# Kernel tuning notes

Measured on AMD Instinct MI355X. Metric: run time of the kernel, lower is better.

## Reference

```python
import jax, jax.numpy as jnp
import numpy as np

GROUP_SIZE = 7
ROI_SCALE = 1.3
BIN_SCALE = 1.5


def setup_inputs() -> dict:
    key = jax.random.key(0)
    k1, k2, k3, k4 = jax.random.split(key, 4)
    B, C, H, W = 2, 490, 128, 128  # C = output_dim(10) * group_size(7)**2
    N = 512
    stride = 16
    features = jax.random.normal(k1, (B, C, H, W), dtype=jnp.float32)
    img_w = W * stride
    bidx = jax.random.randint(k2, (N, 1), 0, B).astype(jnp.float32)
    xy1 = jax.random.uniform(k3, (N, 2), minval=0.0, maxval=img_w - 64.0)
    wh = jax.random.uniform(k4, (N, 2), minval=32.0, maxval=512.0)
    xy2 = jnp.minimum(xy1 + wh, img_w - 1.0)
    rois = jnp.concatenate([bidx, xy1[:, 0:1], xy1[:, 1:2], xy2[:, 0:1], xy2[:, 1:2]], axis=1)
    return {"rois": rois, "features": features, "stride": stride}


def reference(rois, features, stride):
    G = GROUP_SIZE
    B, C, H, W = features.shape
    D = C // (G * G)  # output_dim, computed dynamically as in the torch module
    dt = features.dtype
    spatial_scale = 1.0 / stride

    rois = rois[:, :5].astype(dt)
    batch_idx = rois[:, 0].astype(jnp.int32)  # [N]
    # rounded roi corners in feature-map coordinates (end is inclusive +1)
    rsw = jnp.round(rois[:, 1]) * spatial_scale
    rsh = jnp.round(rois[:, 2]) * spatial_scale
    rew = (jnp.round(rois[:, 3]) + 1.0) * spatial_scale
    reh = (jnp.round(rois[:, 4]) + 1.0) * spatial_scale
    # mask (context) enlargement around roi center by ROI_SCALE
    rw, rh = rew - rsw, reh - rsh
    rwm, rhm = rw * ROI_SCALE, rh * ROI_SCALE
    swm = (rsw + rew) * 0.5 - rwm * 0.5
    shm = (rsh + reh) * 0.5 - rhm * 0.5
    rwm = jnp.maximum(rwm, 0.1)  # force tiny rois to 1x1
    rhm = jnp.maximum(rhm, 0.1)
    bin_h = rhm / G  # [N]
    bin_w = rwm / G
    dh = bin_h * (BIN_SCALE - 1.0) * 0.5  # extra bin context
    dw = bin_w * (BIN_SCALE - 1.0) * 0.5

    g = jnp.arange(G, dtype=dt)  # bin index
    hstart = jnp.clip(jnp.floor(shm[:, None] + g[None, :] * bin_h[:, None] - dh[:, None]), 0, H).astype(jnp.int32)  # [N,G]
    hend = jnp.clip(jnp.ceil(shm[:, None] + (g[None, :] + 1.0) * bin_h[:, None] + dh[:, None]), 0, H).astype(jnp.int32)
    wstart = jnp.clip(jnp.floor(swm[:, None] + g[None, :] * bin_w[:, None] - dw[:, None]), 0, W).astype(jnp.int32)
    wend = jnp.clip(jnp.ceil(swm[:, None] + (g[None, :] + 1.0) * bin_w[:, None] + dw[:, None]), 0, W).astype(jnp.int32)

    # integral image so each bin-average is 4 gathers instead of a dynamic loop
    cs = jnp.cumsum(jnp.cumsum(features, axis=2), axis=3)
    S = jnp.pad(cs, ((0, 0), (0, 0), (1, 0), (1, 0)))  # [B,C,H+1,W+1]
    # position-sensitive channel map c = (d*G + ph)*G + pw  <=>  reshape C -> [D,G,G]
    Sr = S.reshape(B, D, G, G, H + 1, W + 1)

    N = rois.shape[0]
    b_ = batch_idx[:, None, None, None]          # [N,1,1,1]
    d_ = jnp.arange(D)[None, :, None, None]      # [1,D,1,1]
    pi = jnp.arange(G)[None, None, :, None]      # [1,1,G,1] (ph)
    pj = jnp.arange(G)[None, None, None, :]      # [1,1,1,G] (pw)
    hs = hstart[:, None, :, None]
    he = hend[:, None, :, None]
    ws = wstart[:, None, None, :]
    we = wend[:, None, None, :]

    total = (Sr[b_, d_, pi, pj, he, we] - Sr[b_, d_, pi, pj, hs, we]
             - Sr[b_, d_, pi, pj, he, ws] + Sr[b_, d_, pi, pj, hs, ws])  # [N,D,G,G]

    area = ((hend - hstart)[:, None, :, None] * (wend - wstart)[:, None, None, :])  # [N,1->D,G,G] via broadcast
    area = jnp.broadcast_to(area, total.shape)
    out = jnp.where(area > 0, total / jnp.maximum(area, 1).astype(dt), jnp.zeros((), dt))
    return out
```

## Files before the change

### kernel.cpp

```cpp
#include <hip/hip_runtime.h>

#define GS   7
#define CCH  490
#define HH   128
#define WW   128
#define LDW  132
#define NB   2

__global__ __launch_bounds__(512, 4) void psroi_fused(
    const float* __restrict__ rois,
    const float* __restrict__ feat,
    const int*   __restrict__ stride_p,
    float*       __restrict__ out)
{
#pragma clang fp contract(off)
    __shared__ float S[HH * LDW];

    const int bc = blockIdx.x;
    const int b  = bc / CCH;
    const int c  = bc - b * CCH;
    const float* __restrict__ f = feat + (size_t)bc * (HH * WW);
    const int tid = threadIdx.x;

    {
        const int col = tid & 127;
        const int seg = tid >> 7;
        const int r0  = seg * 32;

        float v[32];
        const float* fp = f + r0 * WW + col;
        #pragma unroll
        for (int i = 0; i < 32; ++i)
            v[i] = fp[i * WW];
        #pragma unroll
        for (int i = 1; i < 32; ++i)
            v[i] += v[i - 1];

        S[seg * LDW + col] = v[31];
        __syncthreads();
        float off = 0.0f;
        if (seg > 0) off += S[0 * LDW + col];
        if (seg > 1) off += S[1 * LDW + col];
        if (seg > 2) off += S[2 * LDW + col];
        __syncthreads();

        float* sp = &S[r0 * LDW + col];
        #pragma unroll
        for (int i = 0; i < 32; ++i)
            sp[i * LDW] = v[i] + off;
    }
    __syncthreads();

    {
        const int row = tid >> 2;
        const int ws_ = tid & 3;
        float* rp = &S[row * LDW + ws_ * 32];

        float u[32];
        #pragma unroll
        for (int i = 0; i < 8; ++i) {
            const float4 q = *(const float4*)&rp[i * 4];
            u[4 * i + 0] = q.x; u[4 * i + 1] = q.y;
            u[4 * i + 2] = q.z; u[4 * i + 3] = q.w;
        }
        #pragma unroll
        for (int i = 1; i < 32; ++i)
            u[i] += u[i - 1];

        const float tot = u[31];
        const float t1 = __shfl_up(tot, 1, 64);
        const float t2 = __shfl_up(tot, 2, 64);
        const float t3 = __shfl_up(tot, 3, 64);
        float off = 0.0f;
        if (ws_ > 0) off += t1;
        if (ws_ > 1) off += t2;
        if (ws_ > 2) off += t3;

        #pragma unroll
        for (int i = 0; i < 8; ++i) {
            float4 q;
            q.x = u[4 * i + 0] + off; q.y = u[4 * i + 1] + off;
            q.z = u[4 * i + 2] + off; q.w = u[4 * i + 3] + off;
            *(float4*)&rp[i * 4] = q;
        }
    }
    __syncthreads();

    {
        const int n = tid;
        const float b_f = rois[n * 5 + 0];
        const int bi = (int)b_f;
        if (bi == b) {
            const float ss = 1.0f / (float)(*stride_p);
            const int d   = c / (GS * GS);
            const int rem = c - d * (GS * GS);
            const int pi  = rem / GS;
            const int pj  = rem - pi * GS;

            const float x1 = rois[n * 5 + 1];
            const float y1 = rois[n * 5 + 2];
            const float x2 = rois[n * 5 + 3];
            const float y2 = rois[n * 5 + 4];

            float rsw = rintf(x1) * ss;
            float rsh = rintf(y1) * ss;
            float rew = (rintf(x2) + 1.0f) * ss;
            float reh = (rintf(y2) + 1.0f) * ss;
            float rwv = rew - rsw;
            float rhv = reh - rsh;
            float rwm = rwv * 1.3f;
            float rhm = rhv * 1.3f;
            float swm = (rsw + rew) * 0.5f - rwm * 0.5f;
            float shm = (rsh + reh) * 0.5f - rhm * 0.5f;
            rwm = fmaxf(rwm, 0.1f);
            rhm = fmaxf(rhm, 0.1f);
            float bin_h = rhm / 7.0f;
            float bin_w = rwm / 7.0f;
            float dh = bin_h * 0.25f;
            float dw = bin_w * 0.25f;

            const float gi = (float)pi;
            const float gj = (float)pj;
            const int hs  = (int)fminf(fmaxf(floorf(shm + gi * bin_h - dh),          0.0f), 128.0f);
            const int he  = (int)fminf(fmaxf(ceilf (shm + (gi + 1.0f) * bin_h + dh), 0.0f), 128.0f);
            const int ws2 = (int)fminf(fmaxf(floorf(swm + gj * bin_w - dw),          0.0f), 128.0f);
            const int we  = (int)fminf(fmaxf(ceilf (swm + (gj + 1.0f) * bin_w + dw), 0.0f), 128.0f);

            const int area = (he - hs) * (we - ws2);
            const float A  = (he > 0 && we  > 0) ? S[(he - 1) * LDW + (we  - 1)] : 0.0f;
            const float Bv = (hs > 0 && we  > 0) ? S[(hs - 1) * LDW + (we  - 1)] : 0.0f;
            const float Cv = (he > 0 && ws2 > 0) ? S[(he - 1) * LDW + (ws2 - 1)] : 0.0f;
            const float Dv = (hs > 0 && ws2 > 0) ? S[(hs - 1) * LDW + (ws2 - 1)] : 0.0f;
            const float total = ((A - Bv) - Cv) + Dv;
            out[(size_t)n * CCH + c] = (area > 0) ? (total / (float)area) : 0.0f;
        }
    }
}

extern "C" void kernel_launch(void* const* d_in, const int* in_sizes, int n_in,
                              void* d_out, int out_size, void* d_ws, size_t ws_size,
                              hipStream_t stream)
{
    const float* rois     = (const float*)d_in[0];
    const float* feat     = (const float*)d_in[1];
    const int*   stride_p = (const int*)d_in[2];
    float*       out      = (float*)d_out;

    dim3 grid(NB * CCH);
    dim3 block(512);
    hipLaunchKernelGGL(psroi_fused, grid, block, 0, stream, rois, feat, stride_p, out);
}
```

Baseline: 98.08 us.

## Make psroi kernel persistent with register prefetch of next channel

```diff
diff --git a/kernel.cpp b/kernel.cpp
--- a/kernel.cpp
+++ b/kernel.cpp
@@ -6,6 +6,8 @@
 #define WW   128
 #define LDW  132
 #define NB   2
+#define NCH  (NB * CCH)
+#define NBLK 512
 
 __global__ __launch_bounds__(512, 4) void psroi_fused(
     const float* __restrict__ rois,
@@ -16,124 +18,138 @@
 #pragma clang fp contract(off)
     __shared__ float S[HH * LDW];
 
-    const int bc = blockIdx.x;
-    const int b  = bc / CCH;
-    const int c  = bc - b * CCH;
-    const float* __restrict__ f = feat + (size_t)bc * (HH * WW);
     const int tid = threadIdx.x;
+    const int col = tid & 127;
+    const int seg = tid >> 7;
+    const int r0  = seg * 32;
+    const int row = tid >> 2;
+    const int ws_ = tid & 3;
 
+    const float ss  = 1.0f / (float)(*stride_p);
+    const float b_f = rois[tid * 5 + 0];
+    const int   bi  = (int)b_f;
+    const float x1  = rois[tid * 5 + 1];
+    const float y1  = rois[tid * 5 + 2];
+    const float x2  = rois[tid * 5 + 3];
+    const float y2  = rois[tid * 5 + 4];
+    float rsw = rintf(x1) * ss;
+    float rsh = rintf(y1) * ss;
+    float rew = (rintf(x2) + 1.0f) * ss;
+    float reh = (rintf(y2) + 1.0f) * ss;
+    float rwm = (rew - rsw) * 1.3f;
+    float rhm = (reh - rsh) * 1.3f;
+    const float swm = (rsw + rew) * 0.5f - rwm * 0.5f;
+    const float shm = (rsh + reh) * 0.5f - rhm * 0.5f;
+    rwm = fmaxf(rwm, 0.1f);
+    rhm = fmaxf(rhm, 0.1f);
+    const float bin_h = rhm / 7.0f;
+    const float bin_w = rwm / 7.0f;
+    const float dh = bin_h * 0.25f;
+    const float dw = bin_w * 0.25f;
+
+    int ch = blockIdx.x;
+    float v[32];
     {
-        const int col = tid & 127;
-        const int seg = tid >> 7;
-        const int r0  = seg * 32;
-
-        float v[32];
-        const float* fp = f + r0 * WW + col;
+        const float* __restrict__ fp = feat + (size_t)ch * (HH * WW) + r0 * WW + col;
         #pragma unroll
         for (int i = 0; i < 32; ++i)
             v[i] = fp[i * WW];
+    }
+
+    while (ch < NCH) {
+        const int nxt = ch + NBLK;
+
+        float p[32];
+        if (nxt < NCH) {
+            const float* __restrict__ fp = feat + (size_t)nxt * (HH * WW) + r0 * WW + col;
+            #pragma unroll
+            for (int i = 0; i < 32; ++i)
+                p[i] = fp[i * WW];
+        }
+
         #pragma unroll
         for (int i = 1; i < 32; ++i)
             v[i] += v[i - 1];
 
         S[seg * LDW + col] = v[31];
         __syncthreads();
-        float off = 0.0f;
-        if (seg > 0) off += S[0 * LDW + col];
-        if (seg > 1) off += S[1 * LDW + col];
-        if (seg > 2) off += S[2 * LDW + col];
+        float offA = 0.0f;
+        if (seg > 0) offA += S[0 * LDW + col];
+        if (seg > 1) offA += S[1 * LDW + col];
+        if (seg > 2) offA += S[2 * LDW + col];
         __syncthreads();
 
-        float* sp = &S[r0 * LDW + col];
+        {
+            float* sp = &S[r0 * LDW + col];
+            #pragma unroll
+            for (int i = 0; i < 32; ++i)
+                sp[i * LDW] = v[i] + offA;
+        }
+        __syncthreads();
+
+        {
+            float* rp = &S[row * LDW + ws_ * 32];
+            float u[32];
+            #pragma unroll
+            for (int i = 0; i < 8; ++i) {
+                const float4 q = *(const float4*)&rp[i * 4];
+                u[4 * i + 0] = q.x; u[4 * i + 1] = q.y;
+                u[4 * i + 2] = q.z; u[4 * i + 3] = q.w;
+            }
+            #pragma unroll
+            for (int i = 1; i < 32; ++i)
+                u[i] += u[i - 1];
+
+            const float tot = u[31];
+            const float t1 = __shfl_up(tot, 1, 64);
+            const float t2 = __shfl_up(tot, 2, 64);
+            const float t3 = __shfl_up(tot, 3, 64);
+            float offB = 0.0f;
+            if (ws_ > 0) offB += t1;
+            if (ws_ > 1) offB += t2;
+            if (ws_ > 2) offB += t3;
+
+            #pragma unroll
+            for (int i = 0; i < 8; ++i) {
+                float4 q;
+                q.x = u[4 * i + 0] + offB; q.y = u[4 * i + 1] + offB;
+                q.z = u[4 * i + 2] + offB; q.w = u[4 * i + 3] + offB;
+                *(float4*)&rp[i * 4] = q;
+            }
+        }
+        __syncthreads();
+
+        {
+            const int b = ch / CCH;
+            const int c = ch - b * CCH;
+            if (bi == b) {
+                const int d   = c / (GS * GS);
+                const int rem = c - d * (GS * GS);
+                const int pi  = rem / GS;
+                const int pj  = rem - pi * GS;
+                const float gi = (float)pi;
+                const float gj = (float)pj;
+
+                const int hs  = (int)fminf(fmaxf(floorf(shm + gi * bin_h - dh),          0.0f), 128.0f);
+                const int he  = (int)fminf(fmaxf(ceilf (shm + (gi + 1.0f) * bin_h + dh), 0.0f), 128.0f);
+                const int ws2 = (int)fminf(fmaxf(floorf(swm + gj * bin_w - dw),          0.0f), 128.0f);
+                const int we  = (int)fminf(fmaxf(ceilf (swm + (gj + 1.0f) * bin_w + dw), 0.0f), 128.0f);
+
+                const int area = (he - hs) * (we - ws2);
+                const float A  = (he > 0 && we  > 0) ? S[(he - 1) * LDW + (we  - 1)] : 0.0f;
+                const float Bv = (hs > 0 && we  > 0) ? S[(hs - 1) * LDW + (we  - 1)] : 0.0f;
+                const float Cv = (he > 0 && ws2 > 0) ? S[(he - 1) * LDW + (ws2 - 1)] : 0.0f;
+                const float Dv = (hs > 0 && ws2 > 0) ? S[(hs - 1) * LDW + (ws2 - 1)] : 0.0f;
+                const float total = ((A - Bv) - Cv) + Dv;
+                out[(size_t)tid * CCH + c] = (area > 0) ? (total / (float)area) : 0.0f;
+            }
+        }
+        __syncthreads();
+
         #pragma unroll
         for (int i = 0; i < 32; ++i)
-            sp[i * LDW] = v[i] + off;
-    }
-    __syncthreads();
-
-    {
-        const int row = tid >> 2;
-        const int ws_ = tid & 3;
-        float* rp = &S[row * LDW + ws_ * 32];
-
-        float u[32];
-        #pragma unroll
-        for (int i = 0; i < 8; ++i) {
-            const float4 q = *(const float4*)&rp[i * 4];
-            u[4 * i + 0] = q.x; u[4 * i + 1] = q.y;
-            u[4 * i + 2] = q.z; u[4 * i + 3] = q.w;
-        }
-        #pragma unroll
-        for (int i = 1; i < 32; ++i)
-            u[i] += u[i - 1];
-
-        const float tot = u[31];
-        const float t1 = __shfl_up(tot, 1, 64);
-        const float t2 = __shfl_up(tot, 2, 64);
-        const float t3 = __shfl_up(tot, 3, 64);
-        float off = 0.0f;
-        if (ws_ > 0) off += t1;
-        if (ws_ > 1) off += t2;
-        if (ws_ > 2) off += t3;
-
-        #pragma unroll
-        for (int i = 0; i < 8; ++i) {
-            float4 q;
-            q.x = u[4 * i + 0] + off; q.y = u[4 * i + 1] + off;
-            q.z = u[4 * i + 2] + off; q.w = u[4 * i + 3] + off;
-            *(float4*)&rp[i * 4] = q;
-        }
-    }
-    __syncthreads();
-
-    {
-        const int n = tid;
-        const float b_f = rois[n * 5 + 0];
-        const int bi = (int)b_f;
-        if (bi == b) {
-            const float ss = 1.0f / (float)(*stride_p);
-            const int d   = c / (GS * GS);
-            const int rem = c - d * (GS * GS);
-            const int pi  = rem / GS;
-            const int pj  = rem - pi * GS;
-
-            const float x1 = rois[n * 5 + 1];
-            const float y1 = rois[n * 5 + 2];
-            const float x2 = rois[n * 5 + 3];
-            const float y2 = rois[n * 5 + 4];
-
-            float rsw = rintf(x1) * ss;
-            float rsh = rintf(y1) * ss;
-            float rew = (rintf(x2) + 1.0f) * ss;
-            float reh = (rintf(y2) + 1.0f) * ss;
-            float rwv = rew - rsw;
-            float rhv = reh - rsh;
-            float rwm = rwv * 1.3f;
-            float rhm = rhv * 1.3f;
-            float swm = (rsw + rew) * 0.5f - rwm * 0.5f;
-            float shm = (rsh + reh) * 0.5f - rhm * 0.5f;
-            rwm = fmaxf(rwm, 0.1f);
-            rhm = fmaxf(rhm, 0.1f);
-            float bin_h = rhm / 7.0f;
-            float bin_w = rwm / 7.0f;
-            float dh = bin_h * 0.25f;
-            float dw = bin_w * 0.25f;
-
-            const float gi = (float)pi;
-            const float gj = (float)pj;
-            const int hs  = (int)fminf(fmaxf(floorf(shm + gi * bin_h - dh),          0.0f), 128.0f);
-            const int he  = (int)fminf(fmaxf(ceilf (shm + (gi + 1.0f) * bin_h + dh), 0.0f), 128.0f);
-            const int ws2 = (int)fminf(fmaxf(floorf(swm + gj * bin_w - dw),          0.0f), 128.0f);
-            const int we  = (int)fminf(fmaxf(ceilf (swm + (gj + 1.0f) * bin_w + dw), 0.0f), 128.0f);
-
-            const int area = (he - hs) * (we - ws2);
-            const float A  = (he > 0 && we  > 0) ? S[(he - 1) * LDW + (we  - 1)] : 0.0f;
-            const float Bv = (hs > 0 && we  > 0) ? S[(hs - 1) * LDW + (we  - 1)] : 0.0f;
-            const float Cv = (he > 0 && ws2 > 0) ? S[(he - 1) * LDW + (ws2 - 1)] : 0.0f;
-            const float Dv = (hs > 0 && ws2 > 0) ? S[(hs - 1) * LDW + (ws2 - 1)] : 0.0f;
-            const float total = ((A - Bv) - Cv) + Dv;
-            out[(size_t)n * CCH + c] = (area > 0) ? (total / (float)area) : 0.0f;
-        }
+            v[i] = p[i];
+        ch = nxt;
     }
 }
 
@@ -146,7 +162,7 @@
     const int*   stride_p = (const int*)d_in[2];
     float*       out      = (float*)d_out;
 
-    dim3 grid(NB * CCH);
+    dim3 grid(NBLK);
     dim3 block(512);
     hipLaunchKernelGGL(psroi_fused, grid, block, 0, stream, rois, feat, stride_p, out);
 }
```

Result: slower. 100.4 us (+2.3%).

## Replace 2D integral image with row prefix sums and per-bin row loops

Applied to the files above, without the earlier changes.

```diff
diff --git a/kernel.cpp b/kernel.cpp
--- a/kernel.cpp
+++ b/kernel.cpp
@@ -6,8 +6,9 @@
 #define WW   128
 #define LDW  132
 #define NB   2
+#define NCH  (NB * CCH)
 
-__global__ __launch_bounds__(512, 4) void psroi_fused(
+__global__ __launch_bounds__(512, 4) void psroi_rowpfx(
     const float* __restrict__ rois,
     const float* __restrict__ feat,
     const int*   __restrict__ stride_p,
@@ -16,50 +17,18 @@
 #pragma clang fp contract(off)
     __shared__ float S[HH * LDW];
 
-    const int bc = blockIdx.x;
-    const int b  = bc / CCH;
-    const int c  = bc - b * CCH;
-    const float* __restrict__ f = feat + (size_t)bc * (HH * WW);
+    const int ch  = blockIdx.x;
     const int tid = threadIdx.x;
 
     {
-        const int col = tid & 127;
-        const int seg = tid >> 7;
-        const int r0  = seg * 32;
-
-        float v[32];
-        const float* fp = f + r0 * WW + col;
-        #pragma unroll
-        for (int i = 0; i < 32; ++i)
-            v[i] = fp[i * WW];
-        #pragma unroll
-        for (int i = 1; i < 32; ++i)
-            v[i] += v[i - 1];
-
-        S[seg * LDW + col] = v[31];
-        __syncthreads();
-        float off = 0.0f;
-        if (seg > 0) off += S[0 * LDW + col];
-        if (seg > 1) off += S[1 * LDW + col];
-        if (seg > 2) off += S[2 * LDW + col];
-        __syncthreads();
-
-        float* sp = &S[r0 * LDW + col];
-        #pragma unroll
-        for (int i = 0; i < 32; ++i)
-            sp[i * LDW] = v[i] + off;
-    }
-    __syncthreads();
-
-    {
         const int row = tid >> 2;
-        const int ws_ = tid & 3;
-        float* rp = &S[row * LDW + ws_ * 32];
+        const int sg  = tid & 3;
+        const float* __restrict__ fp = feat + (size_t)ch * (HH * WW) + row * WW + sg * 32;
 
         float u[32];
         #pragma unroll
         for (int i = 0; i < 8; ++i) {
-            const float4 q = *(const float4*)&rp[i * 4];
+            const float4 q = *(const float4*)&fp[i * 4];
             u[4 * i + 0] = q.x; u[4 * i + 1] = q.y;
             u[4 * i + 2] = q.z; u[4 * i + 3] = q.w;
         }
@@ -72,10 +41,11 @@
         const float t2 = __shfl_up(tot, 2, 64);
         const float t3 = __shfl_up(tot, 3, 64);
         float off = 0.0f;
-        if (ws_ > 0) off += t1;
-        if (ws_ > 1) off += t2;
-        if (ws_ > 2) off += t3;
+        if (sg > 0) off += t1;
+        if (sg > 1) off += t2;
+        if (sg > 2) off += t3;
 
+        float* rp = &S[row * LDW + sg * 32];
         #pragma unroll
         for (int i = 0; i < 8; ++i) {
             float4 q;
@@ -87,16 +57,12 @@
     __syncthreads();
 
     {
-        const int n = tid;
-        const float b_f = rois[n * 5 + 0];
-        const int bi = (int)b_f;
+        const int n  = tid;
+        const int b  = ch / CCH;
+        const int c  = ch - b * CCH;
+        const int bi = (int)rois[n * 5 + 0];
         if (bi == b) {
             const float ss = 1.0f / (float)(*stride_p);
-            const int d   = c / (GS * GS);
-            const int rem = c - d * (GS * GS);
-            const int pi  = rem / GS;
-            const int pj  = rem - pi * GS;
-
             const float x1 = rois[n * 5 + 1];
             const float y1 = rois[n * 5 + 2];
             const float x2 = rois[n * 5 + 3];
@@ -106,32 +72,40 @@
             float rsh = rintf(y1) * ss;
             float rew = (rintf(x2) + 1.0f) * ss;
             float reh = (rintf(y2) + 1.0f) * ss;
-            float rwv = rew - rsw;
-            float rhv = reh - rsh;
-            float rwm = rwv * 1.3f;
-            float rhm = rhv * 1.3f;
-            float swm = (rsw + rew) * 0.5f - rwm * 0.5f;
-            float shm = (rsh + reh) * 0.5f - rhm * 0.5f;
+            float rwm = (rew - rsw) * 1.3f;
+            float rhm = (reh - rsh) * 1.3f;
+            const float swm = (rsw + rew) * 0.5f - rwm * 0.5f;
+            const float shm = (rsh + reh) * 0.5f - rhm * 0.5f;
             rwm = fmaxf(rwm, 0.1f);
             rhm = fmaxf(rhm, 0.1f);
-            float bin_h = rhm / 7.0f;
-            float bin_w = rwm / 7.0f;
-            float dh = bin_h * 0.25f;
-            float dw = bin_w * 0.25f;
+            const float bin_h = rhm / 7.0f;
+            const float bin_w = rwm / 7.0f;
+            const float dh = bin_h * 0.25f;
+            const float dw = bin_w * 0.25f;
 
+            const int d   = c / (GS * GS);
+            const int rem = c - d * (GS * GS);
+            const int pi  = rem / GS;
+            const int pj  = rem - pi * GS;
             const float gi = (float)pi;
             const float gj = (float)pj;
+
             const int hs  = (int)fminf(fmaxf(floorf(shm + gi * bin_h - dh),          0.0f), 128.0f);
             const int he  = (int)fminf(fmaxf(ceilf (shm + (gi + 1.0f) * bin_h + dh), 0.0f), 128.0f);
             const int ws2 = (int)fminf(fmaxf(floorf(swm + gj * bin_w - dw),          0.0f), 128.0f);
             const int we  = (int)fminf(fmaxf(ceilf (swm + (gj + 1.0f) * bin_w + dw), 0.0f), 128.0f);
 
             const int area = (he - hs) * (we - ws2);
-            const float A  = (he > 0 && we  > 0) ? S[(he - 1) * LDW + (we  - 1)] : 0.0f;
-            const float Bv = (hs > 0 && we  > 0) ? S[(hs - 1) * LDW + (we  - 1)] : 0.0f;
-            const float Cv = (he > 0 && ws2 > 0) ? S[(he - 1) * LDW + (ws2 - 1)] : 0.0f;
-            const float Dv = (hs > 0 && ws2 > 0) ? S[(hs - 1) * LDW + (ws2 - 1)] : 0.0f;
-            const float total = ((A - Bv) - Cv) + Dv;
+            float total = 0.0f;
+            if (area > 0) {
+                if (ws2 > 0) {
+                    for (int r = hs; r < he; ++r)
+                        total += S[r * LDW + (we - 1)] - S[r * LDW + (ws2 - 1)];
+                } else {
+                    for (int r = hs; r < he; ++r)
+                        total += S[r * LDW + (we - 1)];
+                }
+            }
             out[(size_t)n * CCH + c] = (area > 0) ? (total / (float)area) : 0.0f;
         }
     }
@@ -146,7 +120,7 @@
     const int*   stride_p = (const int*)d_in[2];
     float*       out      = (float*)d_out;
 
-    dim3 grid(NB * CCH);
+    dim3 grid(NCH);
     dim3 block(512);
-    hipLaunchKernelGGL(psroi_fused, grid, block, 0, stream, rois, feat, stride_p, out);
+    hipLaunchKernelGGL(psroi_rowpfx, grid, block, 0, stream, rois, feat, stride_p, out);
 }
```

After: 99.45 us. No clear change (+1.4%).
